# Optimization experiments

Measured on AMD Instinct MI355X. Metric: run time of the kernel, lower is better.

The kernel has to match this reference:

```python
import jax, jax.numpy as jnp
import numpy as np
import random as pyrandom

NUM_CENTERS = 512
NUM_ITERS = 10
EPS = 1e-16
SEED = 42


def setup_inputs() -> dict:
    key = jax.random.key(0)
    x = jax.random.normal(key, (4, 16384, 256), dtype=jnp.float32)
    return {"x": x}


def _get_dist(x, v):
    # squared Euclidean distances: [B, N, K]
    x2 = jnp.sum(x * x, axis=-1, keepdims=True)            # [B, N, 1]
    xv = jnp.einsum('bnd,bkd->bnk', x, v)                  # [B, N, K]
    v2 = jnp.sum(v * v, axis=-1)[:, None, :]               # [B, 1, K]
    return jax.nn.relu(x2 - 2.0 * xv + v2)


def _update_u(x, v):
    clusters = jnp.argmin(_get_dist(x, v), axis=-1)        # [B, N]
    return jax.nn.one_hot(clusters, NUM_CENTERS, dtype=x.dtype)  # [B, N, K]


def _update_v(x, u):
    # normalize memberships over the points axis (torch dim=1 == axis -2 here)
    un = (u + EPS) / (jnp.sum(u, axis=-2, keepdims=True) + EPS)
    return jnp.einsum('bnk,bnd->bkd', un, x)               # [B, K, d]


def reference(x):
    n = x.shape[-2]
    pyrandom.seed(SEED)
    inds = np.asarray(pyrandom.sample(range(n), NUM_CENTERS))
    # initialization happens under no_grad in the original module
    v0 = jax.lax.stop_gradient(x[..., inds, :])            # [B, K, d]
    u0 = jax.lax.stop_gradient(_update_u(x, v0))

    def step(carry, _):
        _, v = carry
        u_new = _update_u(x, v)
        v_new = _update_v(x, u_new)
        return (u_new, v_new), None

    (u, v), _ = jax.lax.scan(step, (u0, v0), None, length=NUM_ITERS)
    return (u, v)
```

## Files before the change

kernel.cpp:

```cpp
#include <hip/hip_runtime.h>
#include <string.h>

#define B 4
#define N 16384
#define D 256
#define K 512
#define ITERS 10

typedef short short8 __attribute__((ext_vector_type(8)));
typedef float float4v __attribute__((ext_vector_type(4)));

static void host_sample_inds(int* out) {
    static unsigned int mt[624];
    mt[0] = 19650218u;
    for (int i = 1; i < 624; i++)
        mt[i] = 1812433253u * (mt[i - 1] ^ (mt[i - 1] >> 30)) + (unsigned)i;
    {
        int i = 1, j = 0;
        for (int kk = 624; kk; kk--) {
            mt[i] = (mt[i] ^ ((mt[i - 1] ^ (mt[i - 1] >> 30)) * 1664525u)) + 42u + (unsigned)j;
            i++; j++;
            if (i >= 624) { mt[0] = mt[623]; i = 1; }
            if (j >= 1) j = 0;
        }
        for (int kk = 623; kk; kk--) {
            mt[i] = (mt[i] ^ ((mt[i - 1] ^ (mt[i - 1] >> 30)) * 1566083941u)) - (unsigned)i;
            i++;
            if (i >= 624) { mt[0] = mt[623]; i = 1; }
        }
        mt[0] = 0x80000000u;
    }
    static unsigned char seen[N];
    memset(seen, 0, sizeof(seen));
    int mti = 624;
    int got = 0;
    while (got < K) {
        if (mti >= 624) {
            for (int kk = 0; kk < 624; kk++) {
                unsigned int yy = (mt[kk] & 0x80000000u) | (mt[(kk + 1) % 624] & 0x7fffffffu);
                mt[kk] = mt[(kk + 397) % 624] ^ (yy >> 1) ^ ((yy & 1u) ? 0x9908b0dfu : 0u);
            }
            mti = 0;
        }
        unsigned int y = mt[mti++];
        y ^= y >> 11; y ^= (y << 7) & 0x9d2c5680u; y ^= (y << 15) & 0xefc60000u; y ^= y >> 18;
        unsigned int r = y >> 17;
        if (r >= (unsigned)N) continue;
        if (seen[r]) continue;
        seen[r] = 1;
        out[got++] = (int)r;
    }
}

__device__ inline void gload_lds16(const void* g, void* l) {
    __builtin_amdgcn_global_load_lds((const __attribute__((address_space(1))) void*)g,
                                     (__attribute__((address_space(3))) void*)l, 16, 0, 0);
}

__device__ inline unsigned bf16_rne(float f) {
    unsigned u = __float_as_uint(f);
    return (u + 0x7fffu + ((u >> 16) & 1u)) >> 16;
}

__device__ inline unsigned long long shfl_xor_u64(unsigned long long v, int off) {
    int lo = __shfl_xor((int)(unsigned)(v & 0xffffffffull), off);
    int hi = __shfl_xor((int)(unsigned)(v >> 32), off);
    return ((unsigned long long)(unsigned)hi << 32) | (unsigned)lo;
}


__global__ void k_gather_v0(const float* __restrict__ x, const int* __restrict__ inds,
                            float* __restrict__ v) {
    int bk = blockIdx.x; int b = bk / K, k = bk % K;
    int n = inds[k];
    const float4* src = (const float4*)(x + ((size_t)b * N + n) * D);
    float4* dst = (float4*)(v + ((size_t)b * K + k) * D);
    dst[threadIdx.x] = src[threadIdx.x];
}

__global__ void k_totsum(const float* __restrict__ x, float* __restrict__ totsum) {
    int b = blockIdx.y;
    int n0 = blockIdx.x * (N / 64);
    int t = threadIdx.x;
    const float* xb = x + (size_t)b * N * D;
    float s = 0.f;
    for (int n = n0; n < n0 + N / 64; n++) s += xb[(size_t)n * D + t];
    atomicAdd(&totsum[b * D + t], s);
}

__global__ void k_prep(const float* __restrict__ src, unsigned short* __restrict__ cat,
                       float* __restrict__ sq, float* __restrict__ resn,
                       float* __restrict__ lon) {
    int wave = threadIdx.x >> 6, lane = threadIdx.x & 63;
    int row = blockIdx.x * 4 + wave;
    float4 f = ((const float4*)(src + (size_t)row * D))[lane];
    float comp[4] = {f.x, f.y, f.z, f.w};
    unsigned short h[4], l[4];
    float r2 = 0.f, l2 = 0.f, n2 = 0.f;
    #pragma unroll
    for (int j = 0; j < 4; j++) {
        n2 += comp[j] * comp[j];
        unsigned hi = bf16_rne(comp[j]);
        float hif = __uint_as_float(hi << 16);
        float r = comp[j] - hif;
        unsigned lo = bf16_rne(r);
        float lof = __uint_as_float(lo << 16);
        float res = r - lof;
        r2 += res * res;
        l2 += lof * lof;
        h[j] = (unsigned short)hi; l[j] = (unsigned short)lo;
    }
    unsigned short* orow = cat + (size_t)row * 512;
    *(ushort4*)&orow[lane * 4] = make_ushort4(h[0], h[1], h[2], h[3]);
    *(ushort4*)&orow[256 + lane * 4] = make_ushort4(l[0], l[1], l[2], l[3]);
    #pragma unroll
    for (int off = 32; off; off >>= 1) {
        r2 += __shfl_xor(r2, off);
        l2 += __shfl_xor(l2, off);
        n2 += __shfl_xor(n2, off);
    }
    if (lane == 0) { sq[row] = n2; resn[row] = sqrtf(r2); lon[row] = sqrtf(l2); }
}

__global__ void k_errmax(const float* __restrict__ v2, const float* __restrict__ vres,
                         const float* __restrict__ vlo,
                         float* __restrict__ vmaxs, float* __restrict__ vresmaxs,
                         float* __restrict__ vlomaxs) {
    __shared__ float s1[256], s2[256], s3[256];
    int b = blockIdx.x, t = threadIdx.x;
    s1[t] = fmaxf(sqrtf(v2[b * K + t]), sqrtf(v2[b * K + 256 + t]));
    s2[t] = fmaxf(vres[b * K + t], vres[b * K + 256 + t]);
    s3[t] = fmaxf(vlo[b * K + t], vlo[b * K + 256 + t]);
    __syncthreads();
    for (int s = 128; s; s >>= 1) {
        if (t < s) {
            s1[t] = fmaxf(s1[t], s1[t + s]);
            s2[t] = fmaxf(s2[t], s2[t + s]);
            s3[t] = fmaxf(s3[t], s3[t + s]);
        }
        __syncthreads();
    }
    if (t == 0) { vmaxs[b] = s1[0]; vresmaxs[b] = s2[0]; vlomaxs[b] = s3[0]; }
}

__global__ void k_transpose(const float* __restrict__ v, float* __restrict__ vT) {
    int idx = blockIdx.x * 256 + threadIdx.x;
    int d = idx & 255, c = (idx >> 8) & 511, b = idx >> 17;
    vT[((size_t)b * D + d) * K + c] = v[idx];
}

__global__ __launch_bounds__(256, 2) void k_gemm_assign(
    const unsigned short* __restrict__ xcat, const unsigned short* __restrict__ vcat,
    const float* __restrict__ x2, const float* __restrict__ v2,
    const float* __restrict__ xres, const float* __restrict__ xlo,
    const float* __restrict__ vmaxs, const float* __restrict__ vresmaxs,
    const float* __restrict__ vlomaxs,
    int* __restrict__ assign, int* __restrict__ counts,
    int* __restrict__ refine_cnt, int* __restrict__ refine_pt) {
    __shared__ __align__(16) unsigned short ringA[4][128 * 32];
    __shared__ __align__(16) unsigned short ringB[4][128 * 32];
    __shared__ float x2s[128];
    __shared__ float v2s[512];
    __shared__ unsigned long long candk[128][2][2];
    int b = blockIdx.y;
    int n0 = blockIdx.x * 128;
    int tid = threadIdx.x;
    int wv = tid >> 6, lane = tid & 63;
    int wr = wv >> 1, wc = wv & 1;
    int quad = lane >> 4, l16 = lane & 15;
    const unsigned short* xb = xcat + ((size_t)b * N + n0) * 512;
    const unsigned short* vb0 = vcat + (size_t)b * K * 512;

    if (tid < 128) x2s[tid] = x2[b * N + n0 + tid];
    v2s[tid] = v2[b * K + tid];
    v2s[tid + 256] = v2[b * K + 256 + tid];

    int ldsoff[2], srow2[2], schunk2[2];
    #pragma unroll
    for (int i = 0; i < 2; i++) {
        int l = i * 256 + tid;
        ldsoff[i] = l * 8;
        srow2[i] = l >> 2;
        schunk2[i] = ((l & 3) ^ ((l >> 3) & 3)) * 8;
    }

    float4v acc[4][4];
    #pragma unroll
    for (int i = 0; i < 4; i++)
        #pragma unroll
        for (int j = 0; j < 4; j++) acc[i][j] = (float4v){0.f, 0.f, 0.f, 0.f};

    unsigned long long k1[16], k2[16];
    #pragma unroll
    for (int i = 0; i < 16; i++) { k1[i] = ~0ull; k2[i] = ~0ull; }

    auto stage_hs = [&](int hs2) {
        int ch2 = hs2 / 24;
        int j2 = hs2 - ch2 * 24;
        int kkt = j2 >> 1, ks = j2 & 1;
        int k4 = ((kkt & 3) << 6) | (ks << 5);
        int kcolA = (kkt < 8) ? k4 : 256 + k4;
        int kcolB = (kkt < 4) ? k4 : ((kkt < 8) ? 256 + k4 : k4);
        const unsigned short* vbn = vb0 + ((size_t)ch2 << 16);
        unsigned short* dA = &ringA[0][0] + ((hs2 & 3) << 12);
        unsigned short* dB = &ringB[0][0] + ((hs2 & 3) << 12);
        #pragma unroll
        for (int i = 0; i < 2; i++) {
            gload_lds16(xb + (size_t)srow2[i] * 512 + kcolA + schunk2[i], dA + ldsoff[i]);
            gload_lds16(vbn + (size_t)srow2[i] * 512 + kcolB + schunk2[i], dB + ldsoff[i]);
        }
    };

    auto compute_hs = [&](int slot) {
        const unsigned short* As_ = &ringA[0][0] + (slot << 12);
        const unsigned short* Bs_ = &ringB[0][0] + (slot << 12);
        short8 af[4], bf[4];
        #pragma unroll
        for (int f = 0; f < 4; f++) {
            int rA = wr * 64 + f * 16 + l16;
            af[f] = *(const short8*)&As_[(rA * 4 + (quad ^ ((rA >> 1) & 3))) * 8];
            int rB = wc * 64 + f * 16 + l16;
            bf[f] = *(const short8*)&Bs_[(rB * 4 + (quad ^ ((rB >> 1) & 3))) * 8];
        }
        __builtin_amdgcn_s_setprio(1);
        #pragma unroll
        for (int fi = 0; fi < 4; fi++)
            #pragma unroll
            for (int fj = 0; fj < 4; fj++)
                acc[fi][fj] = __builtin_amdgcn_mfma_f32_16x16x32_bf16(
                    af[fi], bf[fj], acc[fi][fj], 0, 0, 0);
        __builtin_amdgcn_s_setprio(0);
    };

    auto fold = [&](int ch) {
        #pragma unroll
        for (int fi = 0; fi < 4; fi++) {
            #pragma unroll
            for (int r = 0; r < 4; r++) {
                int lrow = wr * 64 + fi * 16 + quad * 4 + r;
                float x2v = x2s[lrow];
                int idx = fi * 4 + r;
                #pragma unroll
                for (int fj = 0; fj < 4; fj++) {
                    int cg = ch * 128 + wc * 64 + fj * 16 + l16;
                    float dist = fmaxf((x2v - 2.0f * acc[fi][fj][r]) + v2s[cg], 0.0f);
                    unsigned long long key =
                        ((unsigned long long)__float_as_uint(dist) << 32) | (unsigned)cg;
                    if (key < k1[idx]) { k2[idx] = k1[idx]; k1[idx] = key; }
                    else if (key < k2[idx]) { k2[idx] = key; }
                }
            }
        }
        #pragma unroll
        for (int fi = 0; fi < 4; fi++)
            #pragma unroll
            for (int fj = 0; fj < 4; fj++) acc[fi][fj] = (float4v){0.f, 0.f, 0.f, 0.f};
    };

    stage_hs(0); stage_hs(1); stage_hs(2);
    asm volatile("s_waitcnt lgkmcnt(0)" ::: "memory");
    __builtin_amdgcn_s_barrier();

    for (int hs = 0; hs < 93; hs++) {
        asm volatile("s_waitcnt vmcnt(8)" ::: "memory");
        __builtin_amdgcn_s_barrier();
        __builtin_amdgcn_sched_barrier(0);
        stage_hs(hs + 3);
        compute_hs(hs & 3);
        if ((hs % 24) == 23) fold(hs / 24);
    }
    asm volatile("s_waitcnt vmcnt(8)" ::: "memory");
    __builtin_amdgcn_s_barrier();
    __builtin_amdgcn_sched_barrier(0);
    compute_hs(93 & 3);
    asm volatile("s_waitcnt vmcnt(4)" ::: "memory");
    __builtin_amdgcn_s_barrier();
    __builtin_amdgcn_sched_barrier(0);
    compute_hs(94 & 3);
    asm volatile("s_waitcnt vmcnt(0)" ::: "memory");
    __builtin_amdgcn_s_barrier();
    __builtin_amdgcn_sched_barrier(0);
    compute_hs(95 & 3);
    fold(3);

    #pragma unroll
    for (int fi = 0; fi < 4; fi++) {
        #pragma unroll
        for (int r = 0; r < 4; r++) {
            int lrow = wr * 64 + fi * 16 + quad * 4 + r;
            int idx = fi * 4 + r;
            unsigned long long a1 = k1[idx], a2 = k2[idx];
            #pragma unroll
            for (int off = 1; off < 16; off <<= 1) {
                unsigned long long o1 = shfl_xor_u64(a1, off);
                unsigned long long o2 = shfl_xor_u64(a2, off);
                unsigned long long mx = a1 > o1 ? a1 : o1;
                a1 = a1 < o1 ? a1 : o1;
                unsigned long long mn2 = a2 < o2 ? a2 : o2;
                a2 = mx < mn2 ? mx : mn2;
            }
            if (l16 == 0) { candk[lrow][wc][0] = a1; candk[lrow][wc][1] = a2; }
        }
    }
    __syncthreads();
    if (tid < 128) {
        unsigned long long a1 = candk[tid][0][0], a2 = candk[tid][0][1];
        unsigned long long o1 = candk[tid][1][0], o2 = candk[tid][1][1];
        unsigned long long mx = a1 > o1 ? a1 : o1;
        unsigned long long b1 = a1 < o1 ? a1 : o1;
        unsigned long long mn2 = a2 < o2 ? a2 : o2;
        unsigned long long b2 = mx < mn2 ? mx : mn2;
        float bv1 = __uint_as_float((unsigned)(b1 >> 32));
        float bv2 = __uint_as_float((unsigned)(b2 >> 32));
        int bi1 = (int)(unsigned)(b1 & 0xffffffffull);
        int p = b * N + n0 + tid;
        assign[p] = bi1;
        atomicAdd(&counts[b * K + bi1], 1);
        float thr = 4.0f * (xres[p] * vmaxs[b] + sqrtf(x2s[tid]) * vresmaxs[b]
                            + xlo[p] * vlomaxs[b]) + 4e-3f;
        if (bv2 - bv1 < thr) {
            int pos = atomicAdd(refine_cnt, 1);
            refine_pt[pos] = p;
        }
    }
}

__global__ __launch_bounds__(256) void k_rescan(
    const float* __restrict__ x, const float* __restrict__ vT,
    const float* __restrict__ x2, const float* __restrict__ v2,
    const int* __restrict__ refine_cnt, const int* __restrict__ refine_pt,
    int* __restrict__ assign, int* __restrict__ counts) {
    __shared__ float xs[256];
    __shared__ float rv[256];
    __shared__ int ri[256];
    int cnt = *refine_cnt;
    int t = threadIdx.x;
    for (int i = blockIdx.x; i < cnt; i += gridDim.x) {
        int p = refine_pt[i];
        int b = p >> 14;
        xs[t] = x[(size_t)p * D + t];
        __syncthreads();
        const float* vtb = vT + (size_t)b * D * K;
        float s0 = 0.f, s1 = 0.f;
        for (int d = 0; d < D; d++) {
            float xd = xs[d];
            s0 = fmaf(xd, vtb[(size_t)d * K + t], s0);
            s1 = fmaf(xd, vtb[(size_t)d * K + 256 + t], s1);
        }
        float x2p = x2[p];
        float d0 = fmaxf((x2p - 2.0f * s0) + v2[b * K + t], 0.0f);
        float d1 = fmaxf((x2p - 2.0f * s1) + v2[b * K + 256 + t], 0.0f);
        float bv; int bi;
        if (d1 < d0) { bv = d1; bi = t + 256; } else { bv = d0; bi = t; }
        rv[t] = bv; ri[t] = bi;
        __syncthreads();
        for (int s = 128; s; s >>= 1) {
            if (t < s) {
                if (rv[t + s] < rv[t] || (rv[t + s] == rv[t] && ri[t + s] < ri[t])) {
                    rv[t] = rv[t + s]; ri[t] = ri[t + s];
                }
            }
            __syncthreads();
        }
        if (t == 0) {
            int old = assign[p];
            int neu = ri[0];
            if (neu != old) {
                assign[p] = neu;
                atomicSub(&counts[b * K + old], 1);
                atomicAdd(&counts[b * K + neu], 1);
            }
        }
        __syncthreads();
    }
}


__global__ __launch_bounds__(256) void k_scatter(
    const int* __restrict__ assign, const int* __restrict__ counts,
    int* __restrict__ cursor, int* __restrict__ order) {
    __shared__ int offs[K];
    int b = blockIdx.y;
    if (threadIdx.x < 64) {
        int lane = threadIdx.x;
        int pre[8]; int s = 0;
        #pragma unroll
        for (int j = 0; j < 8; j++) { pre[j] = s; s += counts[b * K + lane * 8 + j]; }
        int inc = s;
        #pragma unroll
        for (int off = 1; off < 64; off <<= 1) {
            int o = __shfl_up(inc, off);
            if (lane >= off) inc += o;
        }
        int excl = inc - s;
        #pragma unroll
        for (int j = 0; j < 8; j++) offs[lane * 8 + j] = excl + pre[j];
    }
    __syncthreads();
    int n = blockIdx.x * 256 + threadIdx.x;
    int a = assign[b * N + n];
    int pos = atomicAdd(&cursor[b * K + a], 1);
    order[b * N + offs[a] + pos] = n;
}

__global__ __launch_bounds__(256) void k_sumdiv(
    const float* __restrict__ x, const int* __restrict__ counts,
    const int* __restrict__ order, const float* __restrict__ totsum,
    float* __restrict__ v) {
    __shared__ int sh[256];
    __shared__ int ord[256];
    int t = threadIdx.x;
    int b = blockIdx.y, k = blockIdx.x;
    const int* cb = counts + b * K;
    int partial = 0;
    for (int j = t; j < k; j += 256) partial += cb[j];
    sh[t] = partial; __syncthreads();
    for (int s = 128; s; s >>= 1) { if (t < s) sh[t] += sh[t + s]; __syncthreads(); }
    int off = sh[0];
    int cnt = cb[k];
    const float* xb = x + (size_t)b * N * D;
    float acc = 0.f;
    for (int m0 = 0; m0 < cnt; m0 += 256) {
        int mm = min(256, cnt - m0);
        if (t < mm) ord[t] = order[b * N + off + m0 + t];
        __syncthreads();
        for (int m = 0; m < mm; m++) {
            int n = ord[m];
            acc += xb[(size_t)n * D + t];
        }
        __syncthreads();
    }
    float out;
    if (cnt > 0) out = acc * (1.0f / (float)cnt);
    else out = totsum[b * D + t];
    v[((size_t)b * K + k) * D + t] = out;
}

__global__ void k_write_u(const int* __restrict__ assign, float* __restrict__ uout) {
    int idx = blockIdx.x * 256 + threadIdx.x;
    int a = assign[idx];
    uout[(size_t)idx * K + a] = 1.0f;
}

__global__ void k_copy_v(const float* __restrict__ v, float* __restrict__ out) {
    int idx = blockIdx.x * 256 + threadIdx.x;
    ((float4*)out)[idx] = ((const float4*)v)[idx];
}

extern "C" void kernel_launch(void* const* d_in, const int* in_sizes, int n_in,
                              void* d_out, int out_size, void* d_ws, size_t ws_size,
                              hipStream_t stream) {
    const float* x = (const float*)d_in[0];
    float* out = (float*)d_out;
    char* ws = (char*)d_ws;

    size_t off = 0;
    float* v      = (float*)(ws + off); off += (size_t)B * K * D * 4;
    float* x2     = (float*)(ws + off); off += (size_t)B * N * 4;
    float* v2     = (float*)(ws + off); off += (size_t)B * K * 4;
    float* totsum = (float*)(ws + off); off += (size_t)B * D * 4;
    int* assign   = (int*)(ws + off);   off += (size_t)B * N * 4;
    int* counts   = (int*)(ws + off);   off += (size_t)B * K * 4;
    int* cursor   = (int*)(ws + off);   off += (size_t)B * K * 4;
    int* order    = (int*)(ws + off);   off += (size_t)B * N * 4;
    int* inds     = (int*)(ws + off);   off += 4096;
    int* refine_cnt = (int*)(ws + off); off += 256;

    char* ob = (char*)out;
    size_t oboff = 0;
    unsigned short* xcat = (unsigned short*)(ob + oboff); oboff += (size_t)B * N * 512 * 2;
    int* refine_pt = (int*)(ob + oboff);    oboff += (size_t)B * N * 4;
    float* vT      = (float*)(ob + oboff);  oboff += (size_t)B * K * D * 4;
    float* xres    = (float*)(ob + oboff);  oboff += (size_t)B * N * 4;
    float* xlo     = (float*)(ob + oboff);  oboff += (size_t)B * N * 4;
    float* vres    = (float*)(ob + oboff);  oboff += (size_t)B * K * 4;
    float* vlo     = (float*)(ob + oboff);  oboff += (size_t)B * K * 4;
    float* vmaxs   = (float*)(ob + oboff);  oboff += 256;
    float* vresmaxs = (float*)(ob + oboff); oboff += 256;
    float* vlomaxs = (float*)(ob + oboff);  oboff += 256;
    unsigned short* vcat = (unsigned short*)(out + (size_t)B * N * K);

    static int h_inds[K];
    host_sample_inds(h_inds);
    hipMemcpyAsync(inds, h_inds, K * sizeof(int), hipMemcpyHostToDevice, stream);

    hipMemsetAsync(totsum, 0, (size_t)B * D * 4, stream);
    k_gather_v0<<<B * K, 64, 0, stream>>>(x, inds, v);
    k_totsum<<<dim3(64, B), 256, 0, stream>>>(x, totsum);
    k_prep<<<(B * N) / 4, 256, 0, stream>>>(x, xcat, x2, xres, xlo);

    for (int it = 0; it < ITERS; it++) {
        k_prep<<<(B * K) / 4, 256, 0, stream>>>(v, vcat, v2, vres, vlo);
        k_errmax<<<B, 256, 0, stream>>>(v2, vres, vlo, vmaxs, vresmaxs, vlomaxs);
        k_transpose<<<(B * K * D) / 256, 256, 0, stream>>>(v, vT);
        hipMemsetAsync(refine_cnt, 0, 256, stream);
        hipMemsetAsync(counts, 0, 2 * (size_t)B * K * 4, stream);
        k_gemm_assign<<<dim3(N / 128, B), 256, 0, stream>>>(
            xcat, vcat, x2, v2, xres, xlo, vmaxs, vresmaxs, vlomaxs,
            assign, counts, refine_cnt, refine_pt);
        k_rescan<<<1024, 256, 0, stream>>>(x, vT, x2, v2, refine_cnt, refine_pt,
                                           assign, counts);
        k_scatter<<<dim3(N / 256, B), 256, 0, stream>>>(assign, counts, cursor, order);
        k_sumdiv<<<dim3(K, B), 256, 0, stream>>>(x, counts, order, totsum, v);
    }

    hipMemsetAsync(out, 0, (size_t)B * N * K * 4, stream);
    k_write_u<<<(B * N) / 256, 256, 0, stream>>>(assign, out);
    k_copy_v<<<(B * K * D) / 1024, 256, 0, stream>>>(v, out + (size_t)B * N * K);
}
```

Before: 1.791 ms.

## Enlarge GEMM-assign tile, fuse max reduction and transpose into producers

The distance GEMM kernel now uses 512-thread blocks over 256 points and 256-center chunks, with 8x4 MFMA fragments per wave. Top-2 candidates are reduced across lanes at each fold instead of being kept in per-lane registers. The separate error-max and transpose kernels are removed: k_prep computes the maxima with atomicMax, and k_sumdiv and k_gather_v0 write the transposed centroids directly. The memsets are merged into one, and the totsum and sumdiv loops are unrolled by four. Larger tiles improve operand reuse but raise register pressure and may lower occupancy.

```diff
diff --git a/kernel.cpp b/kernel.cpp
--- a/kernel.cpp
+++ b/kernel.cpp
@@ -70,12 +70,18 @@
 
 
 __global__ void k_gather_v0(const float* __restrict__ x, const int* __restrict__ inds,
-                            float* __restrict__ v) {
+                            float* __restrict__ v, float* __restrict__ vT) {
     int bk = blockIdx.x; int b = bk / K, k = bk % K;
     int n = inds[k];
+    int t = threadIdx.x;
     const float4* src = (const float4*)(x + ((size_t)b * N + n) * D);
     float4* dst = (float4*)(v + ((size_t)b * K + k) * D);
-    dst[threadIdx.x] = src[threadIdx.x];
+    float4 f = src[t];
+    dst[t] = f;
+    float comp[4] = {f.x, f.y, f.z, f.w};
+    #pragma unroll
+    for (int j = 0; j < 4; j++)
+        vT[((size_t)b * D + t * 4 + j) * K + k] = comp[j];
 }
 
 __global__ void k_totsum(const float* __restrict__ x, float* __restrict__ totsum) {
@@ -84,13 +90,21 @@
     int t = threadIdx.x;
     const float* xb = x + (size_t)b * N * D;
     float s = 0.f;
-    for (int n = n0; n < n0 + N / 64; n++) s += xb[(size_t)n * D + t];
+    int n = n0;
+    for (; n + 4 <= n0 + N / 64; n += 4) {
+        float a0 = xb[(size_t)n * D + t];
+        float a1 = xb[(size_t)(n + 1) * D + t];
+        float a2 = xb[(size_t)(n + 2) * D + t];
+        float a3 = xb[(size_t)(n + 3) * D + t];
+        s += a0; s += a1; s += a2; s += a3;
+    }
+    for (; n < n0 + N / 64; n++) s += xb[(size_t)n * D + t];
     atomicAdd(&totsum[b * D + t], s);
 }
 
 __global__ void k_prep(const float* __restrict__ src, unsigned short* __restrict__ cat,
                        float* __restrict__ sq, float* __restrict__ resn,
-                       float* __restrict__ lon) {
+                       float* __restrict__ lon, float* maxbuf) {
     int wave = threadIdx.x >> 6, lane = threadIdx.x & 63;
     int row = blockIdx.x * 4 + wave;
     float4 f = ((const float4*)(src + (size_t)row * D))[lane];
@@ -119,205 +133,186 @@
         l2 += __shfl_xor(l2, off);
         n2 += __shfl_xor(n2, off);
     }
-    if (lane == 0) { sq[row] = n2; resn[row] = sqrtf(r2); lon[row] = sqrtf(l2); }
-}
-
-__global__ void k_errmax(const float* __restrict__ v2, const float* __restrict__ vres,
-                         const float* __restrict__ vlo,
-                         float* __restrict__ vmaxs, float* __restrict__ vresmaxs,
-                         float* __restrict__ vlomaxs) {
-    __shared__ float s1[256], s2[256], s3[256];
-    int b = blockIdx.x, t = threadIdx.x;
-    s1[t] = fmaxf(sqrtf(v2[b * K + t]), sqrtf(v2[b * K + 256 + t]));
-    s2[t] = fmaxf(vres[b * K + t], vres[b * K + 256 + t]);
-    s3[t] = fmaxf(vlo[b * K + t], vlo[b * K + 256 + t]);
-    __syncthreads();
-    for (int s = 128; s; s >>= 1) {
-        if (t < s) {
-            s1[t] = fmaxf(s1[t], s1[t + s]);
-            s2[t] = fmaxf(s2[t], s2[t + s]);
-            s3[t] = fmaxf(s3[t], s3[t + s]);
-        }
-        __syncthreads();
-    }
-    if (t == 0) { vmaxs[b] = s1[0]; vresmaxs[b] = s2[0]; vlomaxs[b] = s3[0]; }
-}
-
-__global__ void k_transpose(const float* __restrict__ v, float* __restrict__ vT) {
-    int idx = blockIdx.x * 256 + threadIdx.x;
-    int d = idx & 255, c = (idx >> 8) & 511, b = idx >> 17;
-    vT[((size_t)b * D + d) * K + c] = v[idx];
-}
-
-__global__ __launch_bounds__(256, 2) void k_gemm_assign(
+    if (lane == 0) {
+        float rn = sqrtf(r2), ln = sqrtf(l2);
+        sq[row] = n2; resn[row] = rn; lon[row] = ln;
+        if (maxbuf) {
+            int b = row >> 9;
+            atomicMax((unsigned int*)&maxbuf[b], __float_as_uint(n2));
+            atomicMax((unsigned int*)&maxbuf[16 + b], __float_as_uint(rn));
+            atomicMax((unsigned int*)&maxbuf[32 + b], __float_as_uint(ln));
+        }
+    }
+}
+
+__global__ __launch_bounds__(512, 2) void k_gemm_assign(
     const unsigned short* __restrict__ xcat, const unsigned short* __restrict__ vcat,
     const float* __restrict__ x2, const float* __restrict__ v2,
     const float* __restrict__ xres, const float* __restrict__ xlo,
-    const float* __restrict__ vmaxs, const float* __restrict__ vresmaxs,
-    const float* __restrict__ vlomaxs,
+    const float* __restrict__ maxbuf,
     int* __restrict__ assign, int* __restrict__ counts,
     int* __restrict__ refine_cnt, int* __restrict__ refine_pt) {
-    __shared__ __align__(16) unsigned short ringA[4][128 * 32];
-    __shared__ __align__(16) unsigned short ringB[4][128 * 32];
-    __shared__ float x2s[128];
+    __shared__ __align__(16) unsigned short ring[4][16384];
+    __shared__ float x2s[256];
     __shared__ float v2s[512];
-    __shared__ unsigned long long candk[128][2][2];
+    __shared__ unsigned long long candk[256][4][2];
     int b = blockIdx.y;
-    int n0 = blockIdx.x * 128;
+    int n0 = blockIdx.x * 256;
     int tid = threadIdx.x;
     int wv = tid >> 6, lane = tid & 63;
-    int wr = wv >> 1, wc = wv & 1;
+    int wr = wv >> 2, wc = wv & 3;
     int quad = lane >> 4, l16 = lane & 15;
     const unsigned short* xb = xcat + ((size_t)b * N + n0) * 512;
     const unsigned short* vb0 = vcat + (size_t)b * K * 512;
 
-    if (tid < 128) x2s[tid] = x2[b * N + n0 + tid];
+    if (tid < 256) x2s[tid] = x2[b * N + n0 + tid];
     v2s[tid] = v2[b * K + tid];
-    v2s[tid + 256] = v2[b * K + 256 + tid];
-
-    int ldsoff[2], srow2[2], schunk2[2];
+
+    int loff[2], srow[2], g8[2];
     #pragma unroll
     for (int i = 0; i < 2; i++) {
-        int l = i * 256 + tid;
-        ldsoff[i] = l * 8;
-        srow2[i] = l >> 2;
-        schunk2[i] = ((l & 3) ^ ((l >> 3) & 3)) * 8;
-    }
-
-    float4v acc[4][4];
+        int l = tid + i * 512;
+        loff[i] = l * 8;
+        srow[i] = l >> 2;
+        g8[i] = (((l & 3) ^ ((l >> 3) & 3))) * 8;
+    }
+
+    float4v acc[8][4];
     #pragma unroll
-    for (int i = 0; i < 4; i++)
+    for (int i = 0; i < 8; i++)
         #pragma unroll
         for (int j = 0; j < 4; j++) acc[i][j] = (float4v){0.f, 0.f, 0.f, 0.f};
 
-    unsigned long long k1[16], k2[16];
-    #pragma unroll
-    for (int i = 0; i < 16; i++) { k1[i] = ~0ull; k2[i] = ~0ull; }
-
-    auto stage_hs = [&](int hs2) {
-        int ch2 = hs2 / 24;
-        int j2 = hs2 - ch2 * 24;
-        int kkt = j2 >> 1, ks = j2 & 1;
-        int k4 = ((kkt & 3) << 6) | (ks << 5);
-        int kcolA = (kkt < 8) ? k4 : 256 + k4;
-        int kcolB = (kkt < 4) ? k4 : ((kkt < 8) ? 256 + k4 : k4);
-        const unsigned short* vbn = vb0 + ((size_t)ch2 << 16);
-        unsigned short* dA = &ringA[0][0] + ((hs2 & 3) << 12);
-        unsigned short* dB = &ringB[0][0] + ((hs2 & 3) << 12);
+    auto stage_u = [&](int u) {
+        int n = u >> 1, ks = u & 1;
+        int ch = n / 12, j = n - ch * 12;
+        int k4 = (j & 3) << 6;
+        int colA = ((j < 8) ? k4 : 256 + k4) + (ks << 5);
+        int colB = ((j < 4) ? k4 : ((j < 8) ? 256 + k4 : k4)) + (ks << 5);
+        const unsigned short* vbn = vb0 + ((size_t)ch << 17);
+        unsigned short* dA = &ring[u & 3][0];
+        unsigned short* dB = &ring[u & 3][8192];
         #pragma unroll
         for (int i = 0; i < 2; i++) {
-            gload_lds16(xb + (size_t)srow2[i] * 512 + kcolA + schunk2[i], dA + ldsoff[i]);
-            gload_lds16(vbn + (size_t)srow2[i] * 512 + kcolB + schunk2[i], dB + ldsoff[i]);
+            gload_lds16(xb + (size_t)srow[i] * 512 + colA + g8[i], dA + loff[i]);
+            gload_lds16(vbn + (size_t)srow[i] * 512 + colB + g8[i], dB + loff[i]);
         }
     };
 
-    auto compute_hs = [&](int slot) {
-        const unsigned short* As_ = &ringA[0][0] + (slot << 12);
-        const unsigned short* Bs_ = &ringB[0][0] + (slot << 12);
-        short8 af[4], bf[4];
-        #pragma unroll
-        for (int f = 0; f < 4; f++) {
-            int rA = wr * 64 + f * 16 + l16;
-            af[f] = *(const short8*)&As_[(rA * 4 + (quad ^ ((rA >> 1) & 3))) * 8];
-            int rB = wc * 64 + f * 16 + l16;
-            bf[f] = *(const short8*)&Bs_[(rB * 4 + (quad ^ ((rB >> 1) & 3))) * 8];
+    auto compute_u = [&](int slot) {
+        const unsigned short* As_ = &ring[slot][0];
+        const unsigned short* Bs_ = &ring[slot][8192];
+        short8 bf[4];
+        #pragma unroll
+        for (int fj = 0; fj < 4; fj++) {
+            int rB = wc * 64 + fj * 16 + l16;
+            bf[fj] = *(const short8*)&Bs_[(rB * 4 + (quad ^ ((rB >> 1) & 3))) * 8];
         }
         __builtin_amdgcn_s_setprio(1);
         #pragma unroll
-        for (int fi = 0; fi < 4; fi++)
+        for (int fi = 0; fi < 8; fi++) {
+            int rA = wr * 128 + fi * 16 + l16;
+            short8 af = *(const short8*)&As_[(rA * 4 + (quad ^ ((rA >> 1) & 3))) * 8];
             #pragma unroll
             for (int fj = 0; fj < 4; fj++)
                 acc[fi][fj] = __builtin_amdgcn_mfma_f32_16x16x32_bf16(
-                    af[fi], bf[fj], acc[fi][fj], 0, 0, 0);
+                    af, bf[fj], acc[fi][fj], 0, 0, 0);
+        }
         __builtin_amdgcn_s_setprio(0);
     };
 
     auto fold = [&](int ch) {
         #pragma unroll
-        for (int fi = 0; fi < 4; fi++) {
+        for (int fi = 0; fi < 8; fi++) {
             #pragma unroll
             for (int r = 0; r < 4; r++) {
-                int lrow = wr * 64 + fi * 16 + quad * 4 + r;
+                int lrow = wr * 128 + fi * 16 + quad * 4 + r;
                 float x2v = x2s[lrow];
-                int idx = fi * 4 + r;
+                unsigned long long t1 = ~0ull, t2 = ~0ull;
                 #pragma unroll
                 for (int fj = 0; fj < 4; fj++) {
-                    int cg = ch * 128 + wc * 64 + fj * 16 + l16;
-                    float dist = fmaxf((x2v - 2.0f * acc[fi][fj][r]) + v2s[cg], 0.0f);
+                    int cg = ch * 256 + wc * 64 + fj * 16 + l16;
+                    float dist = fmaxf((x2v - 2.0f * acc[fi][fj][r]) + v2s[ch ? cg - 256 + 256 : cg], 0.0f);
+                    dist = fmaxf((x2v - 2.0f * acc[fi][fj][r]) + v2s[cg], 0.0f);
                     unsigned long long key =
                         ((unsigned long long)__float_as_uint(dist) << 32) | (unsigned)cg;
-                    if (key < k1[idx]) { k2[idx] = k1[idx]; k1[idx] = key; }
-                    else if (key < k2[idx]) { k2[idx] = key; }
+                    if (key < t1) { t2 = t1; t1 = key; }
+                    else if (key < t2) { t2 = key; }
+                }
+                #pragma unroll
+                for (int off = 1; off < 16; off <<= 1) {
+                    unsigned long long o1 = shfl_xor_u64(t1, off);
+                    unsigned long long o2 = shfl_xor_u64(t2, off);
+                    unsigned long long mx = t1 > o1 ? t1 : o1;
+                    t1 = t1 < o1 ? t1 : o1;
+                    unsigned long long mn2 = t2 < o2 ? t2 : o2;
+                    t2 = mx < mn2 ? mx : mn2;
+                }
+                if (l16 == 0) {
+                    if (ch == 0) {
+                        candk[lrow][wc][0] = t1; candk[lrow][wc][1] = t2;
+                    } else {
+                        unsigned long long a1 = candk[lrow][wc][0], a2 = candk[lrow][wc][1];
+                        unsigned long long mx = a1 > t1 ? a1 : t1;
+                        unsigned long long b1 = a1 < t1 ? a1 : t1;
+                        unsigned long long mn2 = a2 < t2 ? a2 : t2;
+                        unsigned long long b2 = mx < mn2 ? mx : mn2;
+                        candk[lrow][wc][0] = b1; candk[lrow][wc][1] = b2;
+                    }
                 }
             }
         }
         #pragma unroll
-        for (int fi = 0; fi < 4; fi++)
+        for (int fi = 0; fi < 8; fi++)
             #pragma unroll
             for (int fj = 0; fj < 4; fj++) acc[fi][fj] = (float4v){0.f, 0.f, 0.f, 0.f};
     };
 
-    stage_hs(0); stage_hs(1); stage_hs(2);
+    stage_u(0); stage_u(1); stage_u(2);
     asm volatile("s_waitcnt lgkmcnt(0)" ::: "memory");
     __builtin_amdgcn_s_barrier();
 
-    for (int hs = 0; hs < 93; hs++) {
+    for (int u = 0; u < 45; u++) {
         asm volatile("s_waitcnt vmcnt(8)" ::: "memory");
         __builtin_amdgcn_s_barrier();
         __builtin_amdgcn_sched_barrier(0);
-        stage_hs(hs + 3);
-        compute_hs(hs & 3);
-        if ((hs % 24) == 23) fold(hs / 24);
+        stage_u(u + 3);
+        compute_u(u & 3);
+        if (u == 23) fold(0);
     }
     asm volatile("s_waitcnt vmcnt(8)" ::: "memory");
     __builtin_amdgcn_s_barrier();
     __builtin_amdgcn_sched_barrier(0);
-    compute_hs(93 & 3);
+    compute_u(45 & 3);
     asm volatile("s_waitcnt vmcnt(4)" ::: "memory");
     __builtin_amdgcn_s_barrier();
     __builtin_amdgcn_sched_barrier(0);
-    compute_hs(94 & 3);
+    compute_u(46 & 3);
     asm volatile("s_waitcnt vmcnt(0)" ::: "memory");
     __builtin_amdgcn_s_barrier();
     __builtin_amdgcn_sched_barrier(0);
-    compute_hs(95 & 3);
-    fold(3);
-
-    #pragma unroll
-    for (int fi = 0; fi < 4; fi++) {
-        #pragma unroll
-        for (int r = 0; r < 4; r++) {
-            int lrow = wr * 64 + fi * 16 + quad * 4 + r;
-            int idx = fi * 4 + r;
-            unsigned long long a1 = k1[idx], a2 = k2[idx];
-            #pragma unroll
-            for (int off = 1; off < 16; off <<= 1) {
-                unsigned long long o1 = shfl_xor_u64(a1, off);
-                unsigned long long o2 = shfl_xor_u64(a2, off);
-                unsigned long long mx = a1 > o1 ? a1 : o1;
-                a1 = a1 < o1 ? a1 : o1;
-                unsigned long long mn2 = a2 < o2 ? a2 : o2;
-                a2 = mx < mn2 ? mx : mn2;
-            }
-            if (l16 == 0) { candk[lrow][wc][0] = a1; candk[lrow][wc][1] = a2; }
-        }
-    }
+    compute_u(47 & 3);
+    fold(1);
+
     __syncthreads();
-    if (tid < 128) {
-        unsigned long long a1 = candk[tid][0][0], a2 = candk[tid][0][1];
-        unsigned long long o1 = candk[tid][1][0], o2 = candk[tid][1][1];
-        unsigned long long mx = a1 > o1 ? a1 : o1;
-        unsigned long long b1 = a1 < o1 ? a1 : o1;
-        unsigned long long mn2 = a2 < o2 ? a2 : o2;
-        unsigned long long b2 = mx < mn2 ? mx : mn2;
-        float bv1 = __uint_as_float((unsigned)(b1 >> 32));
-        float bv2 = __uint_as_float((unsigned)(b2 >> 32));
-        int bi1 = (int)(unsigned)(b1 & 0xffffffffull);
+    if (tid < 256) {
+        unsigned long long m1 = candk[tid][0][0], m2 = candk[tid][0][1];
+        #pragma unroll
+        for (int g = 1; g < 4; g++) {
+            unsigned long long o1 = candk[tid][g][0], o2 = candk[tid][g][1];
+            unsigned long long mx = m1 > o1 ? m1 : o1;
+            m1 = m1 < o1 ? m1 : o1;
+            unsigned long long mn2 = m2 < o2 ? m2 : o2;
+            m2 = mx < mn2 ? mx : mn2;
+        }
+        float bv1 = __uint_as_float((unsigned)(m1 >> 32));
+        float bv2 = __uint_as_float((unsigned)(m2 >> 32));
+        int bi1 = (int)(unsigned)(m1 & 0xffffffffull);
         int p = b * N + n0 + tid;
         assign[p] = bi1;
         atomicAdd(&counts[b * K + bi1], 1);
-        float thr = 4.0f * (xres[p] * vmaxs[b] + sqrtf(x2s[tid]) * vresmaxs[b]
-                            + xlo[p] * vlomaxs[b]) + 4e-3f;
+        float thr = 4.0f * (xres[p] * sqrtf(maxbuf[b]) + sqrtf(x2s[tid]) * maxbuf[16 + b]
+                            + xlo[p] * maxbuf[32 + b]) + 4e-3f;
         if (bv2 - bv1 < thr) {
             int pos = atomicAdd(refine_cnt, 1);
             refine_pt[pos] = p;
@@ -406,7 +401,7 @@
 __global__ __launch_bounds__(256) void k_sumdiv(
     const float* __restrict__ x, const int* __restrict__ counts,
     const int* __restrict__ order, const float* __restrict__ totsum,
-    float* __restrict__ v) {
+    float* __restrict__ v, float* __restrict__ vT) {
     __shared__ int sh[256];
     __shared__ int ord[256];
     int t = threadIdx.x;
@@ -424,7 +419,16 @@
         int mm = min(256, cnt - m0);
         if (t < mm) ord[t] = order[b * N + off + m0 + t];
         __syncthreads();
-        for (int m = 0; m < mm; m++) {
+        int m = 0;
+        for (; m + 4 <= mm; m += 4) {
+            int i0 = ord[m], i1 = ord[m + 1], i2 = ord[m + 2], i3 = ord[m + 3];
+            float a0 = xb[(size_t)i0 * D + t];
+            float a1 = xb[(size_t)i1 * D + t];
+            float a2 = xb[(size_t)i2 * D + t];
+            float a3 = xb[(size_t)i3 * D + t];
+            acc += a0; acc += a1; acc += a2; acc += a3;
+        }
+        for (; m < mm; m++) {
             int n = ord[m];
             acc += xb[(size_t)n * D + t];
         }
@@ -434,6 +438,7 @@
     if (cnt > 0) out = acc * (1.0f / (float)cnt);
     else out = totsum[b * D + t];
     v[((size_t)b * K + k) * D + t] = out;
+    vT[((size_t)b * D + t) * K + k] = out;
 }
 
 __global__ void k_write_u(const int* __restrict__ assign, float* __restrict__ uout) {
@@ -460,11 +465,13 @@
     float* v2     = (float*)(ws + off); off += (size_t)B * K * 4;
     float* totsum = (float*)(ws + off); off += (size_t)B * D * 4;
     int* assign   = (int*)(ws + off);   off += (size_t)B * N * 4;
+    int* order    = (int*)(ws + off);   off += (size_t)B * N * 4;
+    int* inds     = (int*)(ws + off);   off += 4096;
     int* counts   = (int*)(ws + off);   off += (size_t)B * K * 4;
     int* cursor   = (int*)(ws + off);   off += (size_t)B * K * 4;
-    int* order    = (int*)(ws + off);   off += (size_t)B * N * 4;
-    int* inds     = (int*)(ws + off);   off += 4096;
     int* refine_cnt = (int*)(ws + off); off += 256;
+    float* maxbuf = (float*)(ws + off); off += 256;
+    size_t zero_bytes = 2 * (size_t)B * K * 4 + 512;
 
     char* ob = (char*)out;
     size_t oboff = 0;
@@ -475,9 +482,6 @@
     float* xlo     = (float*)(ob + oboff);  oboff += (size_t)B * N * 4;
     float* vres    = (float*)(ob + oboff);  oboff += (size_t)B * K * 4;
     float* vlo     = (float*)(ob + oboff);  oboff += (size_t)B * K * 4;
-    float* vmaxs   = (float*)(ob + oboff);  oboff += 256;
-    float* vresmaxs = (float*)(ob + oboff); oboff += 256;
-    float* vlomaxs = (float*)(ob + oboff);  oboff += 256;
     unsigned short* vcat = (unsigned short*)(out + (size_t)B * N * K);
 
     static int h_inds[K];
@@ -485,23 +489,20 @@
     hipMemcpyAsync(inds, h_inds, K * sizeof(int), hipMemcpyHostToDevice, stream);
 
     hipMemsetAsync(totsum, 0, (size_t)B * D * 4, stream);
-    k_gather_v0<<<B * K, 64, 0, stream>>>(x, inds, v);
+    k_gather_v0<<<B * K, 64, 0, stream>>>(x, inds, v, vT);
     k_totsum<<<dim3(64, B), 256, 0, stream>>>(x, totsum);
-    k_prep<<<(B * N) / 4, 256, 0, stream>>>(x, xcat, x2, xres, xlo);
+    k_prep<<<(B * N) / 4, 256, 0, stream>>>(x, xcat, x2, xres, xlo, nullptr);
 
     for (int it = 0; it < ITERS; it++) {
-        k_prep<<<(B * K) / 4, 256, 0, stream>>>(v, vcat, v2, vres, vlo);
-        k_errmax<<<B, 256, 0, stream>>>(v2, vres, vlo, vmaxs, vresmaxs, vlomaxs);
-        k_transpose<<<(B * K * D) / 256, 256, 0, stream>>>(v, vT);
-        hipMemsetAsync(refine_cnt, 0, 256, stream);
-        hipMemsetAsync(counts, 0, 2 * (size_t)B * K * 4, stream);
-        k_gemm_assign<<<dim3(N / 128, B), 256, 0, stream>>>(
-            xcat, vcat, x2, v2, xres, xlo, vmaxs, vresmaxs, vlomaxs,
+        hipMemsetAsync(counts, 0, zero_bytes, stream);
+        k_prep<<<(B * K) / 4, 256, 0, stream>>>(v, vcat, v2, vres, vlo, maxbuf);
+        k_gemm_assign<<<dim3(N / 256, B), 512, 0, stream>>>(
+            xcat, vcat, x2, v2, xres, xlo, maxbuf,
             assign, counts, refine_cnt, refine_pt);
         k_rescan<<<1024, 256, 0, stream>>>(x, vT, x2, v2, refine_cnt, refine_pt,
                                            assign, counts);
         k_scatter<<<dim3(N / 256, B), 256, 0, stream>>>(assign, counts, cursor, order);
-        k_sumdiv<<<dim3(K, B), 256, 0, stream>>>(x, counts, order, totsum, v);
+        k_sumdiv<<<dim3(K, B), 256, 0, stream>>>(x, counts, order, totsum, v, vT);
     }
 
     hipMemsetAsync(out, 0, (size_t)B * N * K * 4, stream);
```

New measurement: 2.138 ms. +19.4%, slower.
